# Optimization experiments

Measured on AMD Instinct MI355X. Metric: run time of the kernel, lower is better.

## Reference

```python
import jax, jax.numpy as jnp
import numpy as np
import math

B, S, E, H = 4, 1024, 1024, 16
D = E // H
C = 1.0           # Poincare ball curvature
CS = math.sqrt(C)
EPS = 1e-7

def _sq(x):
    return jnp.sum(x * x, axis=-1, keepdims=True)

def expmap0(v):
    n = jnp.sqrt(jnp.clip(_sq(v), 1e-15))
    return jnp.tanh(CS * n) * v / (CS * n)

def logmap0(y):
    n = jnp.sqrt(jnp.clip(_sq(y), 1e-15))
    t = jnp.clip(CS * n, 0.0, 1.0 - 1e-6)
    return jnp.arctanh(t) * y / (CS * n)

def hlinear(x, z, r):
    # Poincare fully-connected layer (HNN++, Shimizu et al.), as in hypll HLinear
    lam = 2.0 / jnp.clip(1.0 - C * _sq(x), EPS)          # [..., 1] conformal factor
    zn = jnp.clip(jnp.linalg.norm(z, axis=0), 1e-15)     # [out]
    xz = x @ z                                           # [..., out]
    tcr = 2.0 * CS * r
    v = (2.0 * zn / CS) * jnp.arcsinh(CS * lam * xz / zn * jnp.cosh(tcr) - (lam - 1.0) * jnp.sinh(tcr))
    w = jnp.sinh(CS * v) / CS
    return w / (1.0 + jnp.sqrt(1.0 + C * jnp.sum(w * w, -1, keepdims=True)))

def _beta(a, b):
    return math.exp(math.lgamma(a) + math.lgamma(b) - math.lgamma(a + b))

def _forward(query, key, value, zq, bq, zk, bk, zv, bv):
    pq, pk, pv = hlinear(query, zq, bq), hlinear(key, zk, bk), hlinear(value, zv, bv)
    split = lambda x: x.reshape(B, S, H, D).transpose(0, 2, 1, 3)   # [B,H,S,D]
    q, k, v = split(pq), split(pk), split(pv)
    # attention_similarity: negative per-head pairwise Poincare distance (all heads vectorized)
    q2 = jnp.sum(q * q, -1)                              # [B,H,Sq]
    k2 = jnp.sum(k * k, -1)                              # [B,H,Sk]
    qk = jnp.einsum('bhqd,bhkd->bhqk', q, k)
    diff2 = jnp.clip(q2[..., :, None] + k2[..., None, :] - 2.0 * qk, 0.0)
    den = jnp.clip((1.0 - C * q2)[..., :, None] * (1.0 - C * k2)[..., None, :], EPS)
    dist = jnp.arccosh(jnp.clip(1.0 + 2.0 * C * diff2 / den, 1.0 + 1e-6)) / CS
    # attention_activation: softmax over keys
    w = jax.nn.softmax(-dist, axis=-1)                   # [B,H,Sq,Sk]
    # attention_midpoint: weighted gyromidpoint of values over keys
    lam = 2.0 / jnp.clip(1.0 - C * jnp.sum(v * v, -1), EPS)          # [B,H,Sk]
    num = jnp.einsum('bhqk,bhkd->bhqd', w * lam[..., None, :], v)
    dnm = jnp.clip(jnp.einsum('bhqk,bhk->bhq', jnp.abs(w), lam - 1.0), EPS)
    u = num / dnm[..., None]
    mid = u / (1.0 + jnp.sqrt(jnp.clip(1.0 - C * _sq(u), EPS)))      # (1/2) Mobius scalar mult
    # manifold.cat: beta-concatenation of heads (HNN++)
    scale = _beta(E / 2.0, 0.5) / _beta(D / 2.0, 0.5)
    tv = logmap0(mid) * scale                            # tangent at origin, [B,H,S,D]
    return expmap0(tv.transpose(0, 2, 1, 3).reshape(B, S, E))

def setup_inputs():
    key = jax.random.key(0)
    ks = jax.random.split(key, 9)
    mk = lambda k: expmap0(jax.random.normal(k, (B, S, E), jnp.float32) * (0.3 / math.sqrt(E)))
    zs = lambda k: jax.random.normal(k, (E, E), jnp.float32) / math.sqrt(E)
    bs = lambda k: jax.random.normal(k, (E,), jnp.float32) * 0.01
    return {"query": mk(ks[0]), "key": mk(ks[1]), "value": mk(ks[2]),
            "zq": zs(ks[3]), "bq": bs(ks[4]), "zk": zs(ks[5]), "bk": bs(ks[6]),
            "zv": zs(ks[7]), "bv": bs(ks[8])}

def reference(query, key, value, zq, bq, zk, bk, zv, bv):
    return _forward(query, key, value, zq, bq, zk, bk, zv, bv)
```

## Files before the change

### kernel.cpp

```cpp
#include <hip/hip_runtime.h>
#include <cmath>

#define EPSF 1e-7f

constexpr int B_ = 4, S_ = 1024, E_ = 1024, H_ = 16, D_ = 64;
constexpr int BS_ = B_ * S_;

typedef __attribute__((ext_vector_type(8))) short bf16x8;
typedef __attribute__((ext_vector_type(4))) float f32x4;

__device__ inline unsigned int fbits(float f) { union { float f; unsigned int u; } x; x.f = f; return x.u; }
__device__ inline float ubits(unsigned int u) { union { unsigned int u; float f; } x; x.u = u; return x.f; }

__device__ inline unsigned short f2bf(float f) {
  unsigned int u = fbits(f);
  unsigned int r = u + 0x7fffu + ((u >> 16) & 1u);
  return (unsigned short)(r >> 16);
}
__device__ inline float bf2f(unsigned short h) { return ubits(((unsigned int)h) << 16); }
__device__ inline float fastrcp(float x) { return __builtin_amdgcn_rcpf(x); }

__device__ inline unsigned int packhi(float a, float b) {
  return (fbits(a) >> 16) | (fbits(b) & 0xFFFF0000u);
}
__device__ inline unsigned int packlo(float a, float b) {
  float la = a - ubits(fbits(a) & 0xFFFF0000u);
  float lb = b - ubits(fbits(b) & 0xFFFF0000u);
  return (fbits(la) >> 16) | (fbits(lb) & 0xFFFF0000u);
}

__device__ __forceinline__ void async_ld16(const unsigned short* g, unsigned short* l) {
  __builtin_amdgcn_global_load_lds(
      (const __attribute__((address_space(1))) unsigned int*)g,
      (__attribute__((address_space(3))) unsigned int*)l, 16, 0, 0);
}

__global__ __launch_bounds__(256) void xsplit_kernel(
    const float* __restrict__ xq, const float* __restrict__ xk,
    const float* __restrict__ xv, unsigned short* __restrict__ Xbf,
    float* __restrict__ lamRow) {
  const int row = blockIdx.x;
  const float* x = (row < BS_) ? xq : (row < 2 * BS_ ? xk : xv);
  const int r = row & (BS_ - 1);
  const int tid = threadIdx.x;
  float4 v = ((const float4*)(x + (size_t)r * E_))[tid];
  float s = v.x * v.x + v.y * v.y + v.z * v.z + v.w * v.w;
  #pragma unroll
  for (int m = 1; m < 64; m <<= 1) s += __shfl_xor(s, m, 64);
  __shared__ float red[4];
  if ((tid & 63) == 0) red[tid >> 6] = s;
  __syncthreads();
  s = red[0] + red[1] + red[2] + red[3];
  uint2 p;
  p.x = (unsigned int)f2bf(v.x) | ((unsigned int)f2bf(v.y) << 16);
  p.y = (unsigned int)f2bf(v.z) | ((unsigned int)f2bf(v.w) << 16);
  ((uint2*)(Xbf + (size_t)row * E_))[tid] = p;
  if (tid == 0) lamRow[row] = 2.0f / fmaxf(1.0f - s, EPSF);
}

__global__ __launch_bounds__(256) void zsplit_kernel(
    const float* __restrict__ zq, const float* __restrict__ zk, const float* __restrict__ zv,
    unsigned short* __restrict__ BhiT, unsigned short* __restrict__ BloT,
    float* __restrict__ Zpart) {
  const int mat = blockIdx.z;
  const float* z = mat == 0 ? zq : (mat == 1 ? zk : zv);
  const int k0 = blockIdx.y * 64, n0 = blockIdx.x * 64;
  __shared__ float t[64][65];
  __shared__ float sred[64][4];
  const int tid = threadIdx.x;
  {
    int kr = tid >> 4, nc = (tid & 15) * 4;
    #pragma unroll
    for (int i = 0; i < 4; i++) {
      float4 vv = *(const float4*)(z + (size_t)(k0 + kr + i * 16) * E_ + n0 + nc);
      t[kr + i * 16][nc + 0] = vv.x;
      t[kr + i * 16][nc + 1] = vv.y;
      t[kr + i * 16][nc + 2] = vv.z;
      t[kr + i * 16][nc + 3] = vv.w;
    }
  }
  __syncthreads();
  int nr = tid >> 2, kc = (tid & 3) * 16;
  unsigned int ph[8], pl[8];
  float ss = 0.f;
  #pragma unroll
  for (int p = 0; p < 8; p++) {
    float x0 = t[kc + 2 * p][nr], x1 = t[kc + 2 * p + 1][nr];
    ph[p] = packhi(x0, x1);
    pl[p] = packlo(x0, x1);
    ss += x0 * x0 + x1 * x1;
  }
  size_t off = (size_t)mat * E_ * E_ + (size_t)(n0 + nr) * E_ + k0 + kc;
  uint4* dh = (uint4*)(BhiT + off);
  uint4* dl = (uint4*)(BloT + off);
  dh[0] = make_uint4(ph[0], ph[1], ph[2], ph[3]);
  dh[1] = make_uint4(ph[4], ph[5], ph[6], ph[7]);
  dl[0] = make_uint4(pl[0], pl[1], pl[2], pl[3]);
  dl[1] = make_uint4(pl[4], pl[5], pl[6], pl[7]);
  sred[nr][tid & 3] = ss;
  __syncthreads();
  if (tid < 64) {
    float v = sred[tid][0] + sred[tid][1] + sred[tid][2] + sred[tid][3];
    Zpart[(size_t)(mat * 16 + blockIdx.y) * E_ + n0 + tid] = v;
  }
}

__global__ __launch_bounds__(256) void zstat_final_kernel(
    const float* __restrict__ Zpart,
    const float* __restrict__ bq, const float* __restrict__ bk, const float* __restrict__ bv,
    float* __restrict__ znA, float* __restrict__ chA, float* __restrict__ shA) {
  const int idx = blockIdx.x * 256 + threadIdx.x;
  const int mat = idx >> 10, col = idx & 1023;
  const float* bb = mat == 0 ? bq : (mat == 1 ? bk : bv);
  float s = 0.f;
  #pragma unroll
  for (int ky = 0; ky < 16; ky++)
    s += Zpart[(size_t)(mat * 16 + ky) * E_ + col];
  float n = fmaxf(sqrtf(s), 1e-15f);
  znA[idx] = n;
  float rb = bb[col];
  chA[idx] = coshf(2.f * rb);
  shA[idx] = sinhf(2.f * rb);
}

__global__ __launch_bounds__(256, 3) void hlinear_mfma_kernel(
    const unsigned short* __restrict__ Xbf,
    const unsigned short* __restrict__ BhiT, const unsigned short* __restrict__ BloT,
    const float* __restrict__ lamRow, const float* __restrict__ znA,
    const float* __restrict__ chA, const float* __restrict__ shA,
    unsigned short* __restrict__ Wbf) {
  const int mat = blockIdx.z;
  const unsigned short* xa = Xbf + (size_t)mat * BS_ * E_;
  const unsigned short* bh = BhiT + (size_t)mat * E_ * E_;
  const unsigned short* bl = BloT + (size_t)mat * E_ * E_;
  const int lid = blockIdx.y * 8 + blockIdx.x;
  const int sqi = lid >> 4, offb = lid & 15;
  const int m0 = ((sqi >> 1) * 4 + (offb & 3)) * 128;
  const int n0 = ((sqi & 1) * 4 + (offb >> 2)) * 128;

  __shared__ unsigned short LDSU[24576];
  unsigned short* As = LDSU;
  unsigned short* Bh = LDSU + 8192;
  unsigned short* Bl = LDSU + 16384;

  const int tid = threadIdx.x;
  const int wid = tid >> 6, lane = tid & 63, quad = lane >> 4, l16 = lane & 15;
  const int wm = (wid >> 1) * 64, wn = (wid & 1) * 64;

  f32x4 acc[4][4];
  #pragma unroll
  for (int i = 0; i < 4; i++)
    #pragma unroll
    for (int j = 0; j < 4; j++) acc[i][j] = (f32x4){0.f, 0.f, 0.f, 0.f};

  const int lrow = lane >> 3;
  const int lcs = ((lane & 7) ^ lrow) * 8;
  const int xsw = (l16 & 7);

  for (int kt = 0; kt < E_ / 64; ++kt) {
    __syncthreads();
    const int kb = kt * 64 + lcs;
    #pragma unroll
    for (int c2 = 0; c2 < 4; c2++) {
      const int c = wid * 4 + c2;
      const int grow = c * 8 + lrow;
      async_ld16(xa + (size_t)(m0 + grow) * E_ + kb, As + c * 512);
      async_ld16(bh + (size_t)(n0 + grow) * E_ + kb, Bh + c * 512);
      async_ld16(bl + (size_t)(n0 + grow) * E_ + kb, Bl + c * 512);
    }
    __syncthreads();
    #pragma unroll
    for (int h = 0; h < 2; h++) {
      bf16x8 a[4];
      #pragma unroll
      for (int mt = 0; mt < 4; mt++) {
        int row = wm + mt * 16 + l16;
        a[mt] = *(const bf16x8*)&As[row * 64 + (((h * 4 + quad) ^ xsw) * 8)];
      }
      #pragma unroll
      for (int nt = 0; nt < 4; nt++) {
        int row = wn + nt * 16 + l16;
        int ro = row * 64 + (((h * 4 + quad) ^ xsw) * 8);
        bf16x8 bhf = *(const bf16x8*)&Bh[ro];
        bf16x8 blf = *(const bf16x8*)&Bl[ro];
        #pragma unroll
        for (int mt = 0; mt < 4; mt++) {
          acc[mt][nt] = __builtin_amdgcn_mfma_f32_16x16x32_bf16(a[mt], bhf, acc[mt][nt], 0, 0, 0);
          acc[mt][nt] = __builtin_amdgcn_mfma_f32_16x16x32_bf16(a[mt], blf, acc[mt][nt], 0, 0, 0);
        }
      }
    }
  }

  const float* lamP = lamRow + mat * BS_;
  float lamv[16];
  #pragma unroll
  for (int mt = 0; mt < 4; mt++)
    #pragma unroll
    for (int r = 0; r < 4; r++)
      lamv[mt * 4 + r] = lamP[m0 + wm + mt * 16 + quad * 4 + r];

  __syncthreads();
  unsigned short* epi = LDSU + wid * 4608;
  #pragma unroll
  for (int nt = 0; nt < 4; nt++) {
    int cg = n0 + wn + nt * 16 + l16;
    float zn = znA[mat * E_ + cg];
    float chzn = chA[mat * E_ + cg] / zn;
    float sh = shA[mat * E_ + cg];
    float tzn = 2.f * zn;
    #pragma unroll
    for (int mt = 0; mt < 4; mt++) {
      #pragma unroll
      for (int r = 0; r < 4; r++) {
        float lam = lamv[mt * 4 + r];
        float arg = fmaf(lam * acc[mt][nt][r], chzn, -(lam - 1.f) * sh);
        float sq2 = sqrtf(fmaf(arg, arg, 1.f));
        float v = tzn * __logf(arg + sq2);
        float ev = __expf(v);
        float w = 0.5f * (ev - fastrcp(ev));
        epi[(mt * 16 + quad * 4 + r) * 72 + nt * 16 + l16] = f2bf(w);
      }
    }
  }
  unsigned short* gout = Wbf + (size_t)mat * BS_ * E_ + (size_t)(m0 + wm) * E_ + n0 + wn;
  const int rrow = lane >> 3, seg = lane & 7;
  #pragma unroll
  for (int i = 0; i < 8; i++) {
    int row = i * 8 + rrow;
    uint4 val = *(const uint4*)&epi[row * 72 + seg * 8];
    *(uint4*)(gout + (size_t)row * E_ + seg * 8) = val;
  }
}

__global__ __launch_bounds__(256) void normalize_kernel(
    const unsigned short* __restrict__ Wbf, unsigned short* __restrict__ Pbf,
    float* __restrict__ HN) {
  const unsigned short* w = Wbf + (size_t)blockIdx.x * E_;
  int tid = threadIdx.x;
  uint2 wv = ((const uint2*)w)[tid];
  float w0 = bf2f((unsigned short)(wv.x & 0xFFFF));
  float w1 = bf2f((unsigned short)(wv.x >> 16));
  float w2 = bf2f((unsigned short)(wv.y & 0xFFFF));
  float w3 = bf2f((unsigned short)(wv.y >> 16));
  float s = w0 * w0 + w1 * w1 + w2 * w2 + w3 * w3;
  #pragma unroll
  for (int m = 1; m < 64; m <<= 1) s += __shfl_xor(s, m, 64);
  __shared__ float red[4];
  if ((tid & 63) == 0) red[tid >> 6] = s;
  __syncthreads();
  s = red[0] + red[1] + red[2] + red[3];
  float t = 1.f / (1.f + sqrtf(1.f + s));
  unsigned short p0 = f2bf(w0 * t), p1 = f2bf(w1 * t), p2 = f2bf(w2 * t), p3 = f2bf(w3 * t);
  uint2 pk;
  pk.x = (unsigned int)p0 | ((unsigned int)p1 << 16);
  pk.y = (unsigned int)p2 | ((unsigned int)p3 << 16);
  ((uint2*)(Pbf + (size_t)blockIdx.x * E_))[tid] = pk;
  float r0 = bf2f(p0), r1 = bf2f(p1), r2 = bf2f(p2), r3 = bf2f(p3);
  float hs = r0 * r0 + r1 * r1 + r2 * r2 + r3 * r3;
  hs += __shfl_xor(hs, 1, 64);
  hs += __shfl_xor(hs, 2, 64);
  hs += __shfl_xor(hs, 4, 64);
  hs += __shfl_xor(hs, 8, 64);
  if ((tid & 15) == 0) HN[(size_t)blockIdx.x * H_ + (tid >> 4)] = hs;
}

__global__ __launch_bounds__(256) void vtrans_kernel(
    const unsigned short* __restrict__ Pbf, const float* __restrict__ HN,
    unsigned short* __restrict__ VtG, unsigned short* __restrict__ lamMG,
    float* __restrict__ k2T, float* __restrict__ romk2T) {
  const int st = blockIdx.x, h = blockIdx.y, b = blockIdx.z;
  const unsigned short* pv = Pbf + (size_t)2 * BS_ * E_;
  const float* hnk = HN + (size_t)BS_ * H_;
  const float* hnv = HN + (size_t)2 * BS_ * H_;
  __shared__ unsigned short T[64][72];
  __shared__ float lamS[64];
  const int tid = threadIdx.x;
  {
    int lr = tid >> 2, lc = (tid & 3) * 16;
    const uint4* src = (const uint4*)(pv + (size_t)(b * S_ + st * 64 + lr) * E_ + h * 64 + lc);
    *(uint4*)&T[lr][lc] = src[0];
    *(uint4*)&T[lr][lc + 8] = src[1];
  }
  if (tid < 64) {
    float v2 = hnv[(size_t)(b * S_ + st * 64 + tid) * H_ + h];
    float lam = 2.f / fmaxf(1.f - v2, EPSF);
    lamS[tid] = lam;
    size_t sidx = (size_t)(b * H_ + h) * S_ + st * 64 + tid;
    lamMG[sidx] = f2bf(lam - 1.f);
    float k2 = hnk[(size_t)(b * S_ + st * 64 + tid) * H_ + h];
    k2T[sidx] = k2;
    romk2T[sidx] = fastrcp(1.f - k2);
  }
  __syncthreads();
  int d = tid >> 2, sc = (tid & 3) * 16;
  unsigned int o[8];
  #pragma unroll
  for (int i = 0; i < 8; i++) {
    int s0 = sc + 2 * i;
    float f0 = bf2f(T[s0][d]) * lamS[s0];
    float f1 = bf2f(T[s0 + 1][d]) * lamS[s0 + 1];
    o[i] = (unsigned int)f2bf(f0) | ((unsigned int)f2bf(f1) << 16);
  }
  unsigned short* dst = VtG + (size_t)((b * H_ + h) * 64 + d) * S_ + st * 64 + sc;
  ((uint4*)dst)[0] = make_uint4(o[0], o[1], o[2], o[3]);
  ((uint4*)dst)[1] = make_uint4(o[4], o[5], o[6], o[7]);
}

__global__ __launch_bounds__(512) void attention_kernel(
    const unsigned short* __restrict__ Pbf, const float* __restrict__ HN,
    const unsigned short* __restrict__ VtG, const unsigned short* __restrict__ lamMG,
    const float* __restrict__ k2T, const float* __restrict__ romk2T,
    float* __restrict__ TV, float scale) {
  const int qt = blockIdx.x, h = blockIdx.y, b = blockIdx.z;
  const unsigned short* pq = Pbf;
  const unsigned short* pk = Pbf + (size_t)BS_ * E_;
  const float* hnq = HN;

  const int tid = threadIdx.x;
  const int wid = tid >> 6, lane = tid & 63;
  const int quad = lane >> 4, l16 = lane & 15;

  __shared__ __align__(16) unsigned short Kl[4096];
  __shared__ __align__(16) unsigned short Vl[4096];
  __shared__ __align__(16) unsigned short Pw[8][16][72];
  __shared__ __align__(16) float k2L[1024];
  __shared__ __align__(16) float rkL[1024];
  __shared__ __align__(16) unsigned short lamL[1024];

  const size_t bhS = (size_t)(b * H_ + h) * S_;
  ((float2*)k2L)[tid] = ((const float2*)(k2T + bhS))[tid];
  ((float2*)rkL)[tid] = ((const float2*)(romk2T + bhS))[tid];
  ((unsigned int*)lamL)[tid] = ((const unsigned int*)(lamMG + bhS))[tid];

  const int qrow0 = qt * 128 + wid * 16;
  const size_t qgrow = ((size_t)(b * S_ + qrow0 + l16)) * E_ + h * 64;
  bf16x8 aq0 = *(const bf16x8*)(pq + qgrow + quad * 8);
  bf16x8 aq1 = *(const bf16x8*)(pq + qgrow + 32 + quad * 8);
  float q2r[4], tromq2[4];
  #pragma unroll
  for (int r2 = 0; r2 < 4; r2++) {
    float q2 = hnq[((size_t)(b * S_ + qrow0 + quad * 4 + r2)) * H_ + h];
    q2r[r2] = q2;
    tromq2[r2] = 2.f * fastrcp(1.f - q2);
  }

  f32x4 accO[4];
  #pragma unroll
  for (int dt = 0; dt < 4; dt++) accO[dt] = (f32x4){0.f, 0.f, 0.f, 0.f};
  f32x4 accD = (f32x4){0.f, 0.f, 0.f, 0.f};

  const int lr = lane >> 3, cch = lane & 7;
  const int xsw = l16 & 7;
  const unsigned short* kbase = pk + (size_t)(b * S_) * E_ + h * 64;
  const unsigned short* vbase = VtG + bhS * 64;

  for (int kt = 0; kt < S_ / 64; ++kt) {
    __syncthreads();
    {
      const int r = wid * 8 + lr;
      const int cc = ((cch ^ lr) * 8);
      async_ld16(kbase + (size_t)(kt * 64 + r) * E_ + cc, Kl + wid * 512);
      async_ld16(vbase + (size_t)r * S_ + kt * 64 + cc, Vl + wid * 512);
    }
    __syncthreads();

    #pragma unroll
    for (int nt = 0; nt < 4; nt++) {
      const int krow = nt * 16 + l16;
      bf16x8 bk0 = *(const bf16x8*)&Kl[krow * 64 + ((quad ^ xsw) * 8)];
      bf16x8 bk1 = *(const bf16x8*)&Kl[krow * 64 + (((4 + quad) ^ xsw) * 8)];
      f32x4 z = (f32x4){0.f, 0.f, 0.f, 0.f};
      f32x4 d0 = __builtin_amdgcn_mfma_f32_16x16x32_bf16(aq0, bk0, z, 0, 0, 0);
      d0 = __builtin_amdgcn_mfma_f32_16x16x32_bf16(aq1, bk1, d0, 0, 0, 0);
      float k2 = k2L[kt * 64 + krow];
      float romk2 = rkL[kt * 64 + krow];
      #pragma unroll
      for (int r2 = 0; r2 < 4; r2++) {
        float diff2 = fmaf(-2.f, d0[r2], q2r[r2] + k2);
        float t = fmaxf(diff2 * (tromq2[r2] * romk2), 1e-6f);
        float A = 1.f + t;
        float w = A - sqrtf(fmaf(A, A, -1.f));
        Pw[wid][quad * 4 + r2][krow] = (unsigned short)(fbits(w) >> 16);
      }
    }
    bf16x8 ap0 = *(const bf16x8*)&Pw[wid][l16][quad * 8];
    bf16x8 ap1 = *(const bf16x8*)&Pw[wid][l16][32 + quad * 8];
    #pragma unroll
    for (int dt = 0; dt < 4; dt++) {
      const int drow = dt * 16 + l16;
      bf16x8 bv0 = *(const bf16x8*)&Vl[drow * 64 + ((quad ^ xsw) * 8)];
      bf16x8 bv1 = *(const bf16x8*)&Vl[drow * 64 + (((4 + quad) ^ xsw) * 8)];
      accO[dt] = __builtin_amdgcn_mfma_f32_16x16x32_bf16(ap0, bv0, accO[dt], 0, 0, 0);
      accO[dt] = __builtin_amdgcn_mfma_f32_16x16x32_bf16(ap1, bv1, accO[dt], 0, 0, 0);
    }
    bf16x8 bl0 = *(const bf16x8*)&lamL[kt * 64 + quad * 8];
    bf16x8 bl1 = *(const bf16x8*)&lamL[kt * 64 + 32 + quad * 8];
    accD = __builtin_amdgcn_mfma_f32_16x16x32_bf16(ap0, bl0, accD, 0, 0, 0);
    accD = __builtin_amdgcn_mfma_f32_16x16x32_bf16(ap1, bl1, accD, 0, 0, 0);
  }

  #pragma unroll
  for (int r2 = 0; r2 < 4; r2++) {
    float rdsum = 1.f / accD[r2];
    float uu[4];
    float su = 0.f;
    #pragma unroll
    for (int dt = 0; dt < 4; dt++) { uu[dt] = accO[dt][r2] * rdsum; su += uu[dt] * uu[dt]; }
    su += __shfl_xor(su, 1, 64);
    su += __shfl_xor(su, 2, 64);
    su += __shfl_xor(su, 4, 64);
    su += __shfl_xor(su, 8, 64);
    float g = 1.f / (1.f + sqrtf(fmaxf(1.f - su, EPSF)));
    float n2 = fmaxf(su * g * g, 1e-15f);
    float n = sqrtf(n2);
    float fac = atanhf(fminf(n, 1.f - 1e-6f)) / n * g * scale;
    size_t orow = ((size_t)(b * S_ + qrow0 + quad * 4 + r2)) * E_ + h * 64 + l16;
    #pragma unroll
    for (int dt = 0; dt < 4; dt++) TV[orow + dt * 16] = fac * uu[dt];
  }
}

__global__ __launch_bounds__(256) void expmap_kernel(float* __restrict__ TV) {
  float* w = TV + (size_t)blockIdx.x * E_;
  int tid = threadIdx.x;
  float4 v = ((float4*)w)[tid];
  float s = v.x * v.x + v.y * v.y + v.z * v.z + v.w * v.w;
  #pragma unroll
  for (int m = 1; m < 64; m <<= 1) s += __shfl_xor(s, m, 64);
  __shared__ float red[4];
  if ((tid & 63) == 0) red[tid >> 6] = s;
  __syncthreads();
  s = red[0] + red[1] + red[2] + red[3];
  float n = sqrtf(fmaxf(s, 1e-15f));
  float f = tanhf(n) / n;
  v.x *= f; v.y *= f; v.z *= f; v.w *= f;
  ((float4*)w)[tid] = v;
}

extern "C" void kernel_launch(void* const* d_in, const int* in_sizes, int n_in,
                              void* d_out, int out_size, void* d_ws, size_t ws_size,
                              hipStream_t stream) {
  (void)in_sizes; (void)n_in; (void)out_size; (void)ws_size;
  const float* q  = (const float*)d_in[0];
  const float* k  = (const float*)d_in[1];
  const float* v  = (const float*)d_in[2];
  const float* zq = (const float*)d_in[3];
  const float* bq = (const float*)d_in[4];
  const float* zk = (const float*)d_in[5];
  const float* bk = (const float*)d_in[6];
  const float* zv = (const float*)d_in[7];
  const float* bv = (const float*)d_in[8];

  unsigned short* Wbf = (unsigned short*)d_ws;
  unsigned short* Pbf = Wbf + (size_t)3 * BS_ * E_;
  unsigned short* BhiT = Pbf;
  unsigned short* BloT = Pbf + (size_t)3 * E_ * E_;
  unsigned short* Xbf = Pbf + (size_t)3 * BS_ * E_;
  float* HN           = (float*)(Xbf + (size_t)3 * BS_ * E_);
  float* lamRow       = HN + (size_t)3 * BS_ * H_;
  float* znA          = lamRow + 3 * BS_;
  float* chA          = znA + 3 * E_;
  float* shA          = chA + 3 * E_;
  float* Zpart        = shA + 3 * E_;
  unsigned short* VtG = (unsigned short*)(Zpart + 48 * E_);
  unsigned short* lamMG = VtG + (size_t)B_ * H_ * 64 * S_;
  float* k2T          = (float*)(lamMG + (size_t)B_ * H_ * S_);
  float* romk2T       = k2T + (size_t)B_ * H_ * S_;
  float* out          = (float*)d_out;

  double lb1 = lgamma(E_ / 2.0) + lgamma(0.5) - lgamma(E_ / 2.0 + 0.5);
  double lb2 = lgamma(D_ / 2.0) + lgamma(0.5) - lgamma(D_ / 2.0 + 0.5);
  float scale = (float)exp(lb1 - lb2);

  hipLaunchKernelGGL(xsplit_kernel, dim3(3 * BS_), dim3(256), 0, stream, q, k, v, Xbf, lamRow);
  hipLaunchKernelGGL(zsplit_kernel, dim3(16, 16, 3), dim3(256), 0, stream,
                     zq, zk, zv, BhiT, BloT, Zpart);
  hipLaunchKernelGGL(zstat_final_kernel, dim3(12), dim3(256), 0, stream,
                     Zpart, bq, bk, bv, znA, chA, shA);
  hipLaunchKernelGGL(hlinear_mfma_kernel, dim3(8, 32, 3), dim3(256), 0, stream,
                     Xbf, BhiT, BloT, lamRow, znA, chA, shA, Wbf);
  hipLaunchKernelGGL(normalize_kernel, dim3(3 * BS_), dim3(256), 0, stream, Wbf, Pbf, HN);
  hipLaunchKernelGGL(vtrans_kernel, dim3(16, 16, 4), dim3(256), 0, stream,
                     Pbf, HN, VtG, lamMG, k2T, romk2T);
  hipLaunchKernelGGL(attention_kernel, dim3(8, 16, 4), dim3(512), 0, stream,
                     Pbf, HN, VtG, lamMG, k2T, romk2T, out, scale);
  hipLaunchKernelGGL(expmap_kernel, dim3(BS_), dim3(256), 0, stream, out);
}
```

Baseline: 265.3 us.

## Drop split-bf16 weight GEMM and fold distance scaling into QK MFMA

The projection GEMM no longer splits the weights into hi/lo bf16 halves. It uses a single bf16 rounding, which halves the MFMA count and the B-operand loads in that kernel. The attention kernel now pre-scales K by 1/(1-|k|^2) into a contiguous per-head buffer and scales Q by -2*2/(1-|q|^2). An extra rank-2 MFMA injects the q2/k2 terms so the MFMA output is directly the arccosh argument minus one, removing per-element scalar math. This trades accuracy, since the weights lose low-order bits and the norm terms become bf16, for less compute and simpler K tile loads.

```diff
diff --git a/kernel.cpp b/kernel.cpp
--- a/kernel.cpp
+++ b/kernel.cpp
@@ -19,15 +19,6 @@
 }
 __device__ inline float bf2f(unsigned short h) { return ubits(((unsigned int)h) << 16); }
 __device__ inline float fastrcp(float x) { return __builtin_amdgcn_rcpf(x); }
-
-__device__ inline unsigned int packhi(float a, float b) {
-  return (fbits(a) >> 16) | (fbits(b) & 0xFFFF0000u);
-}
-__device__ inline unsigned int packlo(float a, float b) {
-  float la = a - ubits(fbits(a) & 0xFFFF0000u);
-  float lb = b - ubits(fbits(b) & 0xFFFF0000u);
-  return (fbits(la) >> 16) | (fbits(lb) & 0xFFFF0000u);
-}
 
 __device__ __forceinline__ void async_ld16(const unsigned short* g, unsigned short* l) {
   __builtin_amdgcn_global_load_lds(
@@ -60,8 +51,7 @@
 
 __global__ __launch_bounds__(256) void zsplit_kernel(
     const float* __restrict__ zq, const float* __restrict__ zk, const float* __restrict__ zv,
-    unsigned short* __restrict__ BhiT, unsigned short* __restrict__ BloT,
-    float* __restrict__ Zpart) {
+    unsigned short* __restrict__ BhiT, float* __restrict__ Zpart) {
   const int mat = blockIdx.z;
   const float* z = mat == 0 ? zq : (mat == 1 ? zk : zv);
   const int k0 = blockIdx.y * 64, n0 = blockIdx.x * 64;
@@ -81,22 +71,18 @@
   }
   __syncthreads();
   int nr = tid >> 2, kc = (tid & 3) * 16;
-  unsigned int ph[8], pl[8];
+  unsigned int ph[8];
   float ss = 0.f;
   #pragma unroll
   for (int p = 0; p < 8; p++) {
     float x0 = t[kc + 2 * p][nr], x1 = t[kc + 2 * p + 1][nr];
-    ph[p] = packhi(x0, x1);
-    pl[p] = packlo(x0, x1);
+    ph[p] = (unsigned int)f2bf(x0) | ((unsigned int)f2bf(x1) << 16);
     ss += x0 * x0 + x1 * x1;
   }
   size_t off = (size_t)mat * E_ * E_ + (size_t)(n0 + nr) * E_ + k0 + kc;
   uint4* dh = (uint4*)(BhiT + off);
-  uint4* dl = (uint4*)(BloT + off);
   dh[0] = make_uint4(ph[0], ph[1], ph[2], ph[3]);
   dh[1] = make_uint4(ph[4], ph[5], ph[6], ph[7]);
-  dl[0] = make_uint4(pl[0], pl[1], pl[2], pl[3]);
-  dl[1] = make_uint4(pl[4], pl[5], pl[6], pl[7]);
   sred[nr][tid & 3] = ss;
   __syncthreads();
   if (tid < 64) {
@@ -125,23 +111,21 @@
 
 __global__ __launch_bounds__(256, 3) void hlinear_mfma_kernel(
     const unsigned short* __restrict__ Xbf,
-    const unsigned short* __restrict__ BhiT, const unsigned short* __restrict__ BloT,
+    const unsigned short* __restrict__ BhiT,
     const float* __restrict__ lamRow, const float* __restrict__ znA,
     const float* __restrict__ chA, const float* __restrict__ shA,
     unsigned short* __restrict__ Wbf) {
   const int mat = blockIdx.z;
   const unsigned short* xa = Xbf + (size_t)mat * BS_ * E_;
   const unsigned short* bh = BhiT + (size_t)mat * E_ * E_;
-  const unsigned short* bl = BloT + (size_t)mat * E_ * E_;
   const int lid = blockIdx.y * 8 + blockIdx.x;
   const int sqi = lid >> 4, offb = lid & 15;
   const int m0 = ((sqi >> 1) * 4 + (offb & 3)) * 128;
   const int n0 = ((sqi & 1) * 4 + (offb >> 2)) * 128;
 
-  __shared__ unsigned short LDSU[24576];
+  __shared__ unsigned short LDSU[18432];
   unsigned short* As = LDSU;
   unsigned short* Bh = LDSU + 8192;
-  unsigned short* Bl = LDSU + 16384;
 
   const int tid = threadIdx.x;
   const int wid = tid >> 6, lane = tid & 63, quad = lane >> 4, l16 = lane & 15;
@@ -166,7 +150,6 @@
       const int grow = c * 8 + lrow;
       async_ld16(xa + (size_t)(m0 + grow) * E_ + kb, As + c * 512);
       async_ld16(bh + (size_t)(n0 + grow) * E_ + kb, Bh + c * 512);
-      async_ld16(bl + (size_t)(n0 + grow) * E_ + kb, Bl + c * 512);
     }
     __syncthreads();
     #pragma unroll
@@ -180,14 +163,10 @@
       #pragma unroll
       for (int nt = 0; nt < 4; nt++) {
         int row = wn + nt * 16 + l16;
-        int ro = row * 64 + (((h * 4 + quad) ^ xsw) * 8);
-        bf16x8 bhf = *(const bf16x8*)&Bh[ro];
-        bf16x8 blf = *(const bf16x8*)&Bl[ro];
+        bf16x8 bhf = *(const bf16x8*)&Bh[row * 64 + (((h * 4 + quad) ^ xsw) * 8)];
         #pragma unroll
-        for (int mt = 0; mt < 4; mt++) {
+        for (int mt = 0; mt < 4; mt++)
           acc[mt][nt] = __builtin_amdgcn_mfma_f32_16x16x32_bf16(a[mt], bhf, acc[mt][nt], 0, 0, 0);
-          acc[mt][nt] = __builtin_amdgcn_mfma_f32_16x16x32_bf16(a[mt], blf, acc[mt][nt], 0, 0, 0);
-        }
       }
     }
   }
@@ -267,15 +246,17 @@
 
 __global__ __launch_bounds__(256) void vtrans_kernel(
     const unsigned short* __restrict__ Pbf, const float* __restrict__ HN,
-    unsigned short* __restrict__ VtG, unsigned short* __restrict__ lamMG,
-    float* __restrict__ k2T, float* __restrict__ romk2T) {
+    unsigned short* __restrict__ KsG, unsigned short* __restrict__ VtG,
+    unsigned short* __restrict__ lamMG, unsigned int* __restrict__ auxG) {
   const int st = blockIdx.x, h = blockIdx.y, b = blockIdx.z;
+  const unsigned short* pk = Pbf + (size_t)BS_ * E_;
   const unsigned short* pv = Pbf + (size_t)2 * BS_ * E_;
   const float* hnk = HN + (size_t)BS_ * H_;
   const float* hnv = HN + (size_t)2 * BS_ * H_;
   __shared__ unsigned short T[64][72];
-  __shared__ float lamS[64];
+  __shared__ float lamS[64], cS[64];
   const int tid = threadIdx.x;
+  const size_t bhS = (size_t)(b * H_ + h) * S_;
   {
     int lr = tid >> 2, lc = (tid & 3) * 16;
     const uint4* src = (const uint4*)(pv + (size_t)(b * S_ + st * 64 + lr) * E_ + h * 64 + lc);
@@ -286,35 +267,52 @@
     float v2 = hnv[(size_t)(b * S_ + st * 64 + tid) * H_ + h];
     float lam = 2.f / fmaxf(1.f - v2, EPSF);
     lamS[tid] = lam;
-    size_t sidx = (size_t)(b * H_ + h) * S_ + st * 64 + tid;
+    size_t sidx = bhS + st * 64 + tid;
     lamMG[sidx] = f2bf(lam - 1.f);
     float k2 = hnk[(size_t)(b * S_ + st * 64 + tid) * H_ + h];
-    k2T[sidx] = k2;
-    romk2T[sidx] = fastrcp(1.f - k2);
-  }
-  __syncthreads();
-  int d = tid >> 2, sc = (tid & 3) * 16;
-  unsigned int o[8];
-  #pragma unroll
-  for (int i = 0; i < 8; i++) {
-    int s0 = sc + 2 * i;
-    float f0 = bf2f(T[s0][d]) * lamS[s0];
-    float f1 = bf2f(T[s0 + 1][d]) * lamS[s0 + 1];
-    o[i] = (unsigned int)f2bf(f0) | ((unsigned int)f2bf(f1) << 16);
-  }
-  unsigned short* dst = VtG + (size_t)((b * H_ + h) * 64 + d) * S_ + st * 64 + sc;
-  ((uint4*)dst)[0] = make_uint4(o[0], o[1], o[2], o[3]);
-  ((uint4*)dst)[1] = make_uint4(o[4], o[5], o[6], o[7]);
+    float rc = fastrcp(1.f - k2);
+    cS[tid] = rc;
+    auxG[sidx] = (unsigned int)f2bf(rc) | ((unsigned int)f2bf(rc * k2) << 16);
+  }
+  __syncthreads();
+  {
+    int d = tid >> 2, sc = (tid & 3) * 16;
+    unsigned int o[8];
+    #pragma unroll
+    for (int i = 0; i < 8; i++) {
+      int s0 = sc + 2 * i;
+      float f0 = bf2f(T[s0][d]) * lamS[s0];
+      float f1 = bf2f(T[s0 + 1][d]) * lamS[s0 + 1];
+      o[i] = (unsigned int)f2bf(f0) | ((unsigned int)f2bf(f1) << 16);
+    }
+    unsigned short* dst = VtG + (bhS * 64) + (size_t)d * S_ + st * 64 + sc;
+    ((uint4*)dst)[0] = make_uint4(o[0], o[1], o[2], o[3]);
+    ((uint4*)dst)[1] = make_uint4(o[4], o[5], o[6], o[7]);
+  }
+  {
+    int lr = tid >> 2, lc = (tid & 3) * 16;
+    float c = cS[lr];
+    const uint4* src = (const uint4*)(pk + (size_t)(b * S_ + st * 64 + lr) * E_ + h * 64 + lc);
+    union { uint4 q; unsigned short s[8]; } i0, i1, o0, o1;
+    i0.q = src[0]; i1.q = src[1];
+    #pragma unroll
+    for (int j = 0; j < 8; j++) {
+      o0.s[j] = f2bf(bf2f(i0.s[j]) * c);
+      o1.s[j] = f2bf(bf2f(i1.s[j]) * c);
+    }
+    unsigned short* dst = KsG + (bhS + st * 64 + lr) * 64 + lc;
+    ((uint4*)dst)[0] = o0.q;
+    ((uint4*)dst)[1] = o1.q;
+  }
 }
 
 __global__ __launch_bounds__(512) void attention_kernel(
     const unsigned short* __restrict__ Pbf, const float* __restrict__ HN,
-    const unsigned short* __restrict__ VtG, const unsigned short* __restrict__ lamMG,
-    const float* __restrict__ k2T, const float* __restrict__ romk2T,
+    const unsigned short* __restrict__ KsG, const unsigned short* __restrict__ VtG,
+    const unsigned short* __restrict__ lamMG, const unsigned int* __restrict__ auxG,
     float* __restrict__ TV, float scale) {
   const int qt = blockIdx.x, h = blockIdx.y, b = blockIdx.z;
   const unsigned short* pq = Pbf;
-  const unsigned short* pk = Pbf + (size_t)BS_ * E_;
   const float* hnq = HN;
 
   const int tid = threadIdx.x;
@@ -324,26 +322,29 @@
   __shared__ __align__(16) unsigned short Kl[4096];
   __shared__ __align__(16) unsigned short Vl[4096];
   __shared__ __align__(16) unsigned short Pw[8][16][72];
-  __shared__ __align__(16) float k2L[1024];
-  __shared__ __align__(16) float rkL[1024];
   __shared__ __align__(16) unsigned short lamL[1024];
+  __shared__ __align__(16) unsigned int auxL[1024];
 
   const size_t bhS = (size_t)(b * H_ + h) * S_;
-  ((float2*)k2L)[tid] = ((const float2*)(k2T + bhS))[tid];
-  ((float2*)rkL)[tid] = ((const float2*)(romk2T + bhS))[tid];
   ((unsigned int*)lamL)[tid] = ((const unsigned int*)(lamMG + bhS))[tid];
+  ((uint2*)auxL)[tid] = ((const uint2*)(auxG + bhS))[tid];
 
   const int qrow0 = qt * 128 + wid * 16;
   const size_t qgrow = ((size_t)(b * S_ + qrow0 + l16)) * E_ + h * 64;
-  bf16x8 aq0 = *(const bf16x8*)(pq + qgrow + quad * 8);
-  bf16x8 aq1 = *(const bf16x8*)(pq + qgrow + 32 + quad * 8);
-  float q2r[4], tromq2[4];
-  #pragma unroll
-  for (int r2 = 0; r2 < 4; r2++) {
-    float q2 = hnq[((size_t)(b * S_ + qrow0 + quad * 4 + r2)) * H_ + h];
-    q2r[r2] = q2;
-    tromq2[r2] = 2.f * fastrcp(1.f - q2);
-  }
+  bf16x8 aq0r = *(const bf16x8*)(pq + qgrow + quad * 8);
+  bf16x8 aq1r = *(const bf16x8*)(pq + qgrow + 32 + quad * 8);
+  const float q2l = hnq[((size_t)(b * S_ + qrow0 + l16)) * H_ + h];
+  const float al = 2.f * fastrcp(1.f - q2l);
+  const float sc2 = -2.f * al;
+  bf16x8 aq0, aq1;
+  #pragma unroll
+  for (int j = 0; j < 8; j++) {
+    aq0[j] = (short)f2bf(bf2f((unsigned short)aq0r[j]) * sc2);
+    aq1[j] = (short)f2bf(bf2f((unsigned short)aq1r[j]) * sc2);
+  }
+  const unsigned short ae0 = (quad == 0) ? f2bf(al * q2l) : 0;
+  const unsigned short ae1 = (quad == 0) ? f2bf(al) : 0;
+  const bf16x8 aex = (bf16x8){(short)ae0, (short)ae1, 0, 0, 0, 0, 0, 0};
 
   f32x4 accO[4];
   #pragma unroll
@@ -352,7 +353,7 @@
 
   const int lr = lane >> 3, cch = lane & 7;
   const int xsw = l16 & 7;
-  const unsigned short* kbase = pk + (size_t)(b * S_) * E_ + h * 64;
+  const unsigned short* kbase = KsG + bhS * 64;
   const unsigned short* vbase = VtG + bhS * 64;
 
   for (int kt = 0; kt < S_ / 64; ++kt) {
@@ -360,7 +361,7 @@
     {
       const int r = wid * 8 + lr;
       const int cc = ((cch ^ lr) * 8);
-      async_ld16(kbase + (size_t)(kt * 64 + r) * E_ + cc, Kl + wid * 512);
+      async_ld16(kbase + (size_t)(kt * 64 + r) * 64 + cc, Kl + wid * 512);
       async_ld16(vbase + (size_t)r * S_ + kt * 64 + cc, Vl + wid * 512);
     }
     __syncthreads();
@@ -370,15 +371,15 @@
       const int krow = nt * 16 + l16;
       bf16x8 bk0 = *(const bf16x8*)&Kl[krow * 64 + ((quad ^ xsw) * 8)];
       bf16x8 bk1 = *(const bf16x8*)&Kl[krow * 64 + (((4 + quad) ^ xsw) * 8)];
+      unsigned int av = (quad == 0) ? auxL[kt * 64 + krow] : 0u;
+      bf16x8 bex = (bf16x8){(short)(av & 0xFFFF), (short)(av >> 16), 0, 0, 0, 0, 0, 0};
       f32x4 z = (f32x4){0.f, 0.f, 0.f, 0.f};
-      f32x4 d0 = __builtin_amdgcn_mfma_f32_16x16x32_bf16(aq0, bk0, z, 0, 0, 0);
-      d0 = __builtin_amdgcn_mfma_f32_16x16x32_bf16(aq1, bk1, d0, 0, 0, 0);
-      float k2 = k2L[kt * 64 + krow];
-      float romk2 = rkL[kt * 64 + krow];
+      f32x4 st = __builtin_amdgcn_mfma_f32_16x16x32_bf16(aex, bex, z, 0, 0, 0);
+      st = __builtin_amdgcn_mfma_f32_16x16x32_bf16(aq0, bk0, st, 0, 0, 0);
+      st = __builtin_amdgcn_mfma_f32_16x16x32_bf16(aq1, bk1, st, 0, 0, 0);
       #pragma unroll
       for (int r2 = 0; r2 < 4; r2++) {
-        float diff2 = fmaf(-2.f, d0[r2], q2r[r2] + k2);
-        float t = fmaxf(diff2 * (tromq2[r2] * romk2), 1e-6f);
+        float t = fmaxf(st[r2], 1e-6f);
         float A = 1.f + t;
         float w = A - sqrtf(fmaf(A, A, -1.f));
         Pw[wid][quad * 4 + r2][krow] = (unsigned short)(fbits(w) >> 16);
@@ -455,7 +456,6 @@
   unsigned short* Wbf = (unsigned short*)d_ws;
   unsigned short* Pbf = Wbf + (size_t)3 * BS_ * E_;
   unsigned short* BhiT = Pbf;
-  unsigned short* BloT = Pbf + (size_t)3 * E_ * E_;
   unsigned short* Xbf = Pbf + (size_t)3 * BS_ * E_;
   float* HN           = (float*)(Xbf + (size_t)3 * BS_ * E_);
   float* lamRow       = HN + (size_t)3 * BS_ * H_;
@@ -464,9 +464,9 @@
   float* shA          = chA + 3 * E_;
   float* Zpart        = shA + 3 * E_;
   unsigned short* VtG = (unsigned short*)(Zpart + 48 * E_);
-  unsigned short* lamMG = VtG + (size_t)B_ * H_ * 64 * S_;
-  float* k2T          = (float*)(lamMG + (size_t)B_ * H_ * S_);
-  float* romk2T       = k2T + (size_t)B_ * H_ * S_;
+  unsigned short* KsG = VtG + (size_t)B_ * H_ * 64 * S_;
+  unsigned short* lamMG = KsG + (size_t)B_ * H_ * S_ * 64;
+  unsigned int* auxG  = (unsigned int*)(lamMG + (size_t)B_ * H_ * S_);
   float* out          = (float*)d_out;
 
   double lb1 = lgamma(E_ / 2.0) + lgamma(0.5) - lgamma(E_ / 2.0 + 0.5);
@@ -475,15 +475,15 @@
 
   hipLaunchKernelGGL(xsplit_kernel, dim3(3 * BS_), dim3(256), 0, stream, q, k, v, Xbf, lamRow);
   hipLaunchKernelGGL(zsplit_kernel, dim3(16, 16, 3), dim3(256), 0, stream,
-                     zq, zk, zv, BhiT, BloT, Zpart);
+                     zq, zk, zv, BhiT, Zpart);
   hipLaunchKernelGGL(zstat_final_kernel, dim3(12), dim3(256), 0, stream,
                      Zpart, bq, bk, bv, znA, chA, shA);
   hipLaunchKernelGGL(hlinear_mfma_kernel, dim3(8, 32, 3), dim3(256), 0, stream,
-                     Xbf, BhiT, BloT, lamRow, znA, chA, shA, Wbf);
+                     Xbf, BhiT, lamRow, znA, chA, shA, Wbf);
   hipLaunchKernelGGL(normalize_kernel, dim3(3 * BS_), dim3(256), 0, stream, Wbf, Pbf, HN);
   hipLaunchKernelGGL(vtrans_kernel, dim3(16, 16, 4), dim3(256), 0, stream,
-                     Pbf, HN, VtG, lamMG, k2T, romk2T);
+                     Pbf, HN, KsG, VtG, lamMG, auxG);
   hipLaunchKernelGGL(attention_kernel, dim3(8, 16, 4), dim3(512), 0, stream,
-                     Pbf, HN, VtG, lamMG, k2T, romk2T, out, scale);
+                     Pbf, HN, KsG, VtG, lamMG, auxG, out, scale);
   hipLaunchKernelGGL(expmap_kernel, dim3(BS_), dim3(256), 0, stream, out);
 }
```

Measured after the change: 246.9 us. 1.07x faster.
